# Optimization experiments

Measured on AMD Instinct MI355X. Metric: run time of the kernel, lower is better.

## Reference

```python
import jax, jax.numpy as jnp
import numpy as np

N_NODES = 50000
N_EDGES = 800000
N_HEADS = 8
MULT = 16  # multiplicity per degree
F_KEY_NFEAT = MULT * 1 + MULT * 3  # 64


def setup_inputs() -> dict:
    key = jax.random.key(0)
    ks = jax.random.split(key, 7)
    return {
        "v0": jax.random.normal(ks[0], (N_EDGES, MULT, 1), dtype=jnp.float32),
        "v1": jax.random.normal(ks[1], (N_EDGES, MULT, 3), dtype=jnp.float32),
        "k0": jax.random.normal(ks[2], (N_EDGES, MULT, 1), dtype=jnp.float32),
        "k1": jax.random.normal(ks[3], (N_EDGES, MULT, 3), dtype=jnp.float32),
        "q0": jax.random.normal(ks[4], (N_NODES, MULT, 1), dtype=jnp.float32),
        "q1": jax.random.normal(ks[5], (N_NODES, MULT, 3), dtype=jnp.float32),
        "edge_index": jax.random.randint(ks[6], (2, N_EDGES), 0, N_NODES, dtype=jnp.int32),
    }


def _fiber2head(d0, d1, n_heads):
    # [X, m, 2d+1] -> [X, H, (m/H)*(2d+1)], concat over degrees on last axis
    x0 = d0.reshape(d0.shape[0], n_heads, -1)
    x1 = d1.reshape(d1.shape[0], n_heads, -1)
    return jnp.concatenate([x0, x1], axis=-1)


def reference(v0, v1, k0, k1, q0, q1, edge_index):
    row, col = edge_index[0], edge_index[1]
    N = q0.shape[0]
    H = N_HEADS

    k = _fiber2head(k0, k1, H)          # [E, H, 8]
    q = _fiber2head(q0, q1, H)          # [N, H, 8]

    # per-edge attention logits (dot over channel dim), scaled by sqrt(f_key.n_features)
    e = (k * q[col]).sum(axis=2) / np.float32(np.sqrt(F_KEY_NFEAT))  # [E, H]
    e = jnp.exp(e)
    s = jax.ops.segment_sum(e, row, num_segments=N)  # [N, H]
    a = e / s[row]                                   # [E, H]
    attn = a[:, :, None, None]                       # [E, H, 1, 1]

    mH = MULT // H
    # degree-0 messages: [E, H, m/H, 1]
    out0 = jax.ops.segment_sum(attn * v0.reshape(-1, H, mH, 1), col, num_segments=N)
    out0 = out0.reshape(N, MULT, 1)
    # degree-1 messages: [E, H, m/H, 3]
    out1 = jax.ops.segment_sum(attn * v1.reshape(-1, H, mH, 3), col, num_segments=N)
    out1 = out1.reshape(N, MULT, 3)
    return out0, out1
```

## Files before the change

### kernel.cpp

```cpp
#include <hip/hip_runtime.h>
#include <hip/hip_fp16.h>

#define N_NODES 50000
#define N_EDGES 800000

struct alignas(16) H8 { __half h[8]; };

__global__ __launch_bounds__(256) void k_hist(const int* __restrict__ ei,
                                              int* __restrict__ cnt_c)
{
    int e = blockIdx.x * blockDim.x + threadIdx.x;
    if (e >= N_EDGES) return;
    atomicAdd(cnt_c + ei[N_EDGES + e], 1);
}

#define SCAN_T 1024
#define SCAN_I 8
__global__ __launch_bounds__(SCAN_T) void k_scan(int* cnt, int* off)
{
    __shared__ int sm[SCAN_T];
    __shared__ int carry_s;
    const int n = N_NODES;
    if (threadIdx.x == 0) carry_s = 0;
    __syncthreads();
    for (int base = 0; base < n; base += SCAN_T * SCAN_I) {
        int idx0 = base + threadIdx.x * SCAN_I;
        int v[SCAN_I];
        int sum = 0;
        #pragma unroll
        for (int j = 0; j < SCAN_I; ++j) {
            int i = idx0 + j;
            v[j] = (i < n) ? cnt[i] : 0;
            sum += v[j];
        }
        sm[threadIdx.x] = sum;
        __syncthreads();
        for (int d = 1; d < SCAN_T; d <<= 1) {
            int t = (threadIdx.x >= d) ? sm[threadIdx.x - d] : 0;
            __syncthreads();
            sm[threadIdx.x] += t;
            __syncthreads();
        }
        int excl_thread = sm[threadIdx.x] - sum;
        int carry = carry_s;
        int run = carry + excl_thread;
        #pragma unroll
        for (int j = 0; j < SCAN_I; ++j) {
            int i = idx0 + j;
            if (i < n) { off[i] = run; cnt[i] = run; }
            run += v[j];
        }
        __syncthreads();
        if (threadIdx.x == SCAN_T - 1) carry_s = carry + sm[threadIdx.x];
        __syncthreads();
    }
    if (threadIdx.x == 0) off[n] = carry_s;
}

__global__ __launch_bounds__(256) void k_logits_fill(
    const float* __restrict__ k0, const float* __restrict__ k1,
    const float* __restrict__ q0, const float* __restrict__ q1,
    const int* __restrict__ ei, __half* __restrict__ e_buf,
    float* __restrict__ s,
    int* __restrict__ cur_c, int* __restrict__ eid_c)
{
    int e = blockIdx.x * blockDim.x + threadIdx.x;
    if (e >= N_EDGES) return;
    int row = ei[e];
    int col = ei[N_EDGES + e];

    const float4* k0v = (const float4*)(k0 + (size_t)e   * 16);
    const float4* q0v = (const float4*)(q0 + (size_t)col * 16);
    const float4* k1v = (const float4*)(k1 + (size_t)e   * 48);
    const float4* q1v = (const float4*)(q1 + (size_t)col * 48);

    float acc[8];
    #pragma unroll
    for (int h = 0; h < 8; ++h) acc[h] = 0.f;

    #pragma unroll
    for (int i = 0; i < 4; ++i) {
        float4 kv = k0v[i];
        float4 qv = q0v[i];
        acc[(4*i+0)/2] += kv.x * qv.x;
        acc[(4*i+1)/2] += kv.y * qv.y;
        acc[(4*i+2)/2] += kv.z * qv.z;
        acc[(4*i+3)/2] += kv.w * qv.w;
    }
    #pragma unroll
    for (int j = 0; j < 12; ++j) {
        float4 kv = k1v[j];
        float4 qv = q1v[j];
        acc[(4*j+0)/6] += kv.x * qv.x;
        acc[(4*j+1)/6] += kv.y * qv.y;
        acc[(4*j+2)/6] += kv.z * qv.z;
        acc[(4*j+3)/6] += kv.w * qv.w;
    }

    H8 pack;
    #pragma unroll
    for (int h = 0; h < 8; ++h) {
        __half hv = __float2half(__expf(acc[h] * 0.125f));
        pack.h[h] = hv;
        atomicAdd(s + (size_t)row * 8 + h, __half2float(hv));
    }
    *(H8*)(e_buf + (size_t)e * 8) = pack;

    int pc = atomicAdd(cur_c + col, 1);
    eid_c[pc] = e;
}

__global__ __launch_bounds__(256) void k_rs(const float* __restrict__ s,
                                            float* __restrict__ rs)
{
    int i = blockIdx.x * blockDim.x + threadIdx.x;
    if (i < N_NODES * 8) rs[i] = 1.0f / s[i];
}

__global__ __launch_bounds__(256) void k_out(
    const float* __restrict__ v0, const float* __restrict__ v1,
    const int* __restrict__ ei, const __half* __restrict__ e_buf,
    const float* __restrict__ rs,
    const int* __restrict__ off_c, const int* __restrict__ eid_c,
    float* __restrict__ out0, float* __restrict__ out1)
{
    int wave = (blockIdx.x * blockDim.x + threadIdx.x) >> 6;
    int lane = threadIdx.x & 63;
    if (wave >= N_NODES) return;
    bool is0 = lane < 16;
    int f1 = lane - 16;
    int head = is0 ? (lane >> 1) : (f1 / 6);
    const float* __restrict__ vbase = is0 ? (v0 + lane) : (v1 + f1);
    int vstride = is0 ? 16 : 48;

    int beg = off_c[wave], end = off_c[wave + 1];
    float acc = 0.f;
    int i = beg;
    for (; i + 4 <= end; i += 4) {
        int e0 = eid_c[i + 0];
        int e1 = eid_c[i + 1];
        int e2 = eid_c[i + 2];
        int e3 = eid_c[i + 3];
        int r0 = ei[e0], r1 = ei[e1], r2 = ei[e2], r3 = ei[e3];
        float w0 = vbase[(size_t)e0 * vstride];
        float w1 = vbase[(size_t)e1 * vstride];
        float w2 = vbase[(size_t)e2 * vstride];
        float w3 = vbase[(size_t)e3 * vstride];
        float a0 = __half2float(e_buf[(size_t)e0 * 8 + head]) * rs[(size_t)r0 * 8 + head];
        float a1 = __half2float(e_buf[(size_t)e1 * 8 + head]) * rs[(size_t)r1 * 8 + head];
        float a2 = __half2float(e_buf[(size_t)e2 * 8 + head]) * rs[(size_t)r2 * 8 + head];
        float a3 = __half2float(e_buf[(size_t)e3 * 8 + head]) * rs[(size_t)r3 * 8 + head];
        acc += a0 * w0;
        acc += a1 * w1;
        acc += a2 * w2;
        acc += a3 * w3;
    }
    for (; i < end; ++i) {
        int e0 = eid_c[i];
        int r0 = ei[e0];
        acc += __half2float(e_buf[(size_t)e0 * 8 + head])
             * rs[(size_t)r0 * 8 + head]
             * vbase[(size_t)e0 * vstride];
    }
    if (is0) out0[(size_t)wave * 16 + lane] = acc;
    else     out1[(size_t)wave * 48 + f1]   = acc;
}

extern "C" void kernel_launch(void* const* d_in, const int* in_sizes, int n_in,
                              void* d_out, int out_size, void* d_ws, size_t ws_size,
                              hipStream_t stream) {
    const float* v0 = (const float*)d_in[0];
    const float* v1 = (const float*)d_in[1];
    const float* k0 = (const float*)d_in[2];
    const float* k1 = (const float*)d_in[3];
    const float* q0 = (const float*)d_in[4];
    const float* q1 = (const float*)d_in[5];
    const int*   ei = (const int*)d_in[6];

    float* out0 = (float*)d_out;
    float* out1 = out0 + (size_t)N_NODES * 16;

    char* ws = (char*)d_ws;
    float*  s     = (float*) (ws + 0);
    int*    cnt_c = (int*)   (ws + 1600000);
    int*    off_c = (int*)   (ws + 1800000);
    int*    eid_c = (int*)   (ws + 2000016);
    __half* e_buf = (__half*)(ws + 5200016);
    float*  rs    = (float*) (ws + 18000016);

    hipMemsetAsync(ws, 0, 1800000, stream);

    const int block = 256;
    const int gridE = (N_EDGES + block - 1) / block;

    k_hist<<<gridE, block, 0, stream>>>(ei, cnt_c);
    k_scan<<<1, SCAN_T, 0, stream>>>(cnt_c, off_c);
    k_logits_fill<<<gridE, block, 0, stream>>>(k0, k1, q0, q1, ei, e_buf,
                                               s, cnt_c, eid_c);
    k_rs<<<(N_NODES * 8 + block - 1) / block, block, 0, stream>>>(s, rs);
    k_out<<<(N_NODES * 64 + block - 1) / block, block, 0, stream>>>(
        v0, v1, ei, e_buf, rs, off_c, eid_c, out0, out1);
}
```

Before: 861.7 us.

## Replace float atomic softmax-denominator accumulation with row-CSR gather reduction

Builds a second CSR keyed by source row (histogram, scan and fill) and computes each node's per-head softmax denominator by gathering exp-logits in a new kernel, instead of eight float atomicAdds per edge. It aims to remove 6.4M contended float atomics from the logits kernel. In exchange it adds another int atomic per edge, a second serial scan pass, an extra 3.2MB index array, and a gather kernel with uncoalesced 2-byte loads.

```diff
diff --git a/kernel.cpp b/kernel.cpp
--- a/kernel.cpp
+++ b/kernel.cpp
@@ -7,67 +7,78 @@
 struct alignas(16) H8 { __half h[8]; };
 
 __global__ __launch_bounds__(256) void k_hist(const int* __restrict__ ei,
+                                              int* __restrict__ cnt_r,
                                               int* __restrict__ cnt_c)
 {
     int e = blockIdx.x * blockDim.x + threadIdx.x;
     if (e >= N_EDGES) return;
+    atomicAdd(cnt_r + ei[e], 1);
     atomicAdd(cnt_c + ei[N_EDGES + e], 1);
 }
 
 #define SCAN_T 1024
 #define SCAN_I 8
-__global__ __launch_bounds__(SCAN_T) void k_scan(int* cnt, int* off)
+__global__ __launch_bounds__(SCAN_T) void k_scan2(int* cnt_r, int* off_r,
+                                                  int* cnt_c, int* off_c)
 {
     __shared__ int sm[SCAN_T];
     __shared__ int carry_s;
     const int n = N_NODES;
-    if (threadIdx.x == 0) carry_s = 0;
-    __syncthreads();
-    for (int base = 0; base < n; base += SCAN_T * SCAN_I) {
-        int idx0 = base + threadIdx.x * SCAN_I;
-        int v[SCAN_I];
-        int sum = 0;
-        #pragma unroll
-        for (int j = 0; j < SCAN_I; ++j) {
-            int i = idx0 + j;
-            v[j] = (i < n) ? cnt[i] : 0;
-            sum += v[j];
-        }
-        sm[threadIdx.x] = sum;
+    for (int pass = 0; pass < 2; ++pass) {
+        int* cnt = pass ? cnt_c : cnt_r;
+        int* off = pass ? off_c : off_r;
+        if (threadIdx.x == 0) carry_s = 0;
         __syncthreads();
-        for (int d = 1; d < SCAN_T; d <<= 1) {
-            int t = (threadIdx.x >= d) ? sm[threadIdx.x - d] : 0;
+        for (int base = 0; base < n; base += SCAN_T * SCAN_I) {
+            int idx0 = base + threadIdx.x * SCAN_I;
+            int v[SCAN_I];
+            int sum = 0;
+            #pragma unroll
+            for (int j = 0; j < SCAN_I; ++j) {
+                int i = idx0 + j;
+                v[j] = (i < n) ? cnt[i] : 0;
+                sum += v[j];
+            }
+            sm[threadIdx.x] = sum;
             __syncthreads();
-            sm[threadIdx.x] += t;
+            for (int d = 1; d < SCAN_T; d <<= 1) {
+                int t = (threadIdx.x >= d) ? sm[threadIdx.x - d] : 0;
+                __syncthreads();
+                sm[threadIdx.x] += t;
+                __syncthreads();
+            }
+            int excl_thread = sm[threadIdx.x] - sum;
+            int carry = carry_s;
+            int run = carry + excl_thread;
+            #pragma unroll
+            for (int j = 0; j < SCAN_I; ++j) {
+                int i = idx0 + j;
+                if (i < n) { off[i] = run; cnt[i] = run; }
+                run += v[j];
+            }
+            __syncthreads();
+            if (threadIdx.x == SCAN_T - 1) carry_s = carry + sm[threadIdx.x];
             __syncthreads();
         }
-        int excl_thread = sm[threadIdx.x] - sum;
-        int carry = carry_s;
-        int run = carry + excl_thread;
-        #pragma unroll
-        for (int j = 0; j < SCAN_I; ++j) {
-            int i = idx0 + j;
-            if (i < n) { off[i] = run; cnt[i] = run; }
-            run += v[j];
-        }
+        if (threadIdx.x == 0) off[n] = carry_s;
         __syncthreads();
-        if (threadIdx.x == SCAN_T - 1) carry_s = carry + sm[threadIdx.x];
-        __syncthreads();
-    }
-    if (threadIdx.x == 0) off[n] = carry_s;
+    }
 }
 
 __global__ __launch_bounds__(256) void k_logits_fill(
     const float* __restrict__ k0, const float* __restrict__ k1,
     const float* __restrict__ q0, const float* __restrict__ q1,
     const int* __restrict__ ei, __half* __restrict__ e_buf,
-    float* __restrict__ s,
-    int* __restrict__ cur_c, int* __restrict__ eid_c)
+    int* __restrict__ cur_r, int* __restrict__ cur_c,
+    int* __restrict__ eid_r, int* __restrict__ eid_c)
 {
     int e = blockIdx.x * blockDim.x + threadIdx.x;
     if (e >= N_EDGES) return;
     int row = ei[e];
     int col = ei[N_EDGES + e];
+
+    int pr = atomicAdd(cur_r + row, 1);
+    int pc = atomicAdd(cur_c + col, 1);
 
     const float4* k0v = (const float4*)(k0 + (size_t)e   * 16);
     const float4* q0v = (const float4*)(q0 + (size_t)col * 16);
@@ -99,22 +110,40 @@
 
     H8 pack;
     #pragma unroll
-    for (int h = 0; h < 8; ++h) {
-        __half hv = __float2half(__expf(acc[h] * 0.125f));
-        pack.h[h] = hv;
-        atomicAdd(s + (size_t)row * 8 + h, __half2float(hv));
-    }
+    for (int h = 0; h < 8; ++h) pack.h[h] = __float2half(__expf(acc[h] * 0.125f));
     *(H8*)(e_buf + (size_t)e * 8) = pack;
 
-    int pc = atomicAdd(cur_c + col, 1);
+    eid_r[pr] = e;
     eid_c[pc] = e;
 }
 
-__global__ __launch_bounds__(256) void k_rs(const float* __restrict__ s,
-                                            float* __restrict__ rs)
-{
-    int i = blockIdx.x * blockDim.x + threadIdx.x;
-    if (i < N_NODES * 8) rs[i] = 1.0f / s[i];
+__global__ __launch_bounds__(256) void k_s(const __half* __restrict__ e_buf,
+                                           const int* __restrict__ off_r,
+                                           const int* __restrict__ eid_r,
+                                           float* __restrict__ rs)
+{
+    int t = blockIdx.x * blockDim.x + threadIdx.x;
+    int node = t >> 3;
+    int h = t & 7;
+    if (node >= N_NODES) return;
+    int beg = off_r[node], end = off_r[node + 1];
+    float acc = 0.f;
+    int i = beg;
+    for (; i + 4 <= end; i += 4) {
+        int e0 = eid_r[i + 0];
+        int e1 = eid_r[i + 1];
+        int e2 = eid_r[i + 2];
+        int e3 = eid_r[i + 3];
+        float x0 = __half2float(e_buf[(size_t)e0 * 8 + h]);
+        float x1 = __half2float(e_buf[(size_t)e1 * 8 + h]);
+        float x2 = __half2float(e_buf[(size_t)e2 * 8 + h]);
+        float x3 = __half2float(e_buf[(size_t)e3 * 8 + h]);
+        acc += x0; acc += x1; acc += x2; acc += x3;
+    }
+    for (; i < end; ++i) {
+        acc += __half2float(e_buf[(size_t)eid_r[i] * 8 + h]);
+    }
+    rs[(size_t)node * 8 + h] = 1.0f / acc;
 }
 
 __global__ __launch_bounds__(256) void k_out(
@@ -181,23 +210,25 @@
     float* out1 = out0 + (size_t)N_NODES * 16;
 
     char* ws = (char*)d_ws;
-    float*  s     = (float*) (ws + 0);
-    int*    cnt_c = (int*)   (ws + 1600000);
-    int*    off_c = (int*)   (ws + 1800000);
-    int*    eid_c = (int*)   (ws + 2000016);
-    __half* e_buf = (__half*)(ws + 5200016);
-    float*  rs    = (float*) (ws + 18000016);
-
-    hipMemsetAsync(ws, 0, 1800000, stream);
+    int*    cnt_r = (int*)   (ws + 0);
+    int*    cnt_c = (int*)   (ws + 200000);
+    int*    off_r = (int*)   (ws + 400000);
+    int*    off_c = (int*)   (ws + 600016);
+    int*    eid_r = (int*)   (ws + 800032);
+    int*    eid_c = (int*)   (ws + 4000032);
+    __half* e_buf = (__half*)(ws + 7200032);
+    float*  rs    = (float*) (ws + 20000032);
+
+    hipMemsetAsync(cnt_r, 0, 400000, stream);
 
     const int block = 256;
     const int gridE = (N_EDGES + block - 1) / block;
 
-    k_hist<<<gridE, block, 0, stream>>>(ei, cnt_c);
-    k_scan<<<1, SCAN_T, 0, stream>>>(cnt_c, off_c);
+    k_hist<<<gridE, block, 0, stream>>>(ei, cnt_r, cnt_c);
+    k_scan2<<<1, SCAN_T, 0, stream>>>(cnt_r, off_r, cnt_c, off_c);
     k_logits_fill<<<gridE, block, 0, stream>>>(k0, k1, q0, q1, ei, e_buf,
-                                               s, cnt_c, eid_c);
-    k_rs<<<(N_NODES * 8 + block - 1) / block, block, 0, stream>>>(s, rs);
+                                               cnt_r, cnt_c, eid_r, eid_c);
+    k_s<<<(N_NODES * 8 + block - 1) / block, block, 0, stream>>>(e_buf, off_r, eid_r, rs);
     k_out<<<(N_NODES * 64 + block - 1) / block, block, 0, stream>>>(
         v0, v1, ei, e_buf, rs, off_c, eid_c, out0, out1);
 }
```

Result: faster. 734.2 us (-14.8%).
